# Optimization experiments

Hardware: AMD Instinct MI355X
Metric: run time of the kernel (lower is better)

## Reference

```python
import jax, jax.numpy as jnp
import numpy as np

EPS = 1e-5  # BatchNorm2d default eps


def _squash(s, axis):
    # s * (|s|^2 / ((1+|s|^2) * |s|)) == s * |s| / (1 + |s|^2)
    n = jnp.linalg.norm(s, axis=axis, keepdims=True)
    return s * (n / (1.0 + n * n))


def _bn(y, g, b, m, v):
    # eval-mode batchnorm with running stats, broadcast over channel axis
    return (y - m) * (g * jax.lax.rsqrt(v + EPS)) + b


def setup_inputs() -> dict:
    key = jax.random.key(0)
    ks = jax.random.split(key, 18)
    B, N = 4, 2048
    f32 = jnp.float32
    return {
        "x": jax.random.normal(ks[0], (B, N, 3), f32),
        "w1": 0.1 * jax.random.normal(ks[1], (64, 3), f32),
        "g1": jax.random.uniform(ks[2], (64,), f32) + 0.5,
        "b1": 0.1 * jax.random.normal(ks[3], (64,), f32),
        "m1": 0.1 * jax.random.normal(ks[4], (64,), f32),
        "v1": jax.random.uniform(ks[5], (64,), f32) + 0.5,
        "w2": 0.05 * jax.random.normal(ks[6], (128, 64), f32),
        "g2": jax.random.uniform(ks[7], (128,), f32) + 0.5,
        "b2": 0.1 * jax.random.normal(ks[8], (128,), f32),
        "m2": 0.1 * jax.random.normal(ks[9], (128,), f32),
        "v2": jax.random.uniform(ks[10], (128,), f32) + 0.5,
        "wb": 0.05 * jax.random.normal(ks[11], (16, 1024, 128), f32),
        "gb": jax.random.uniform(ks[12], (16, 1024), f32) + 0.5,
        "bb": 0.1 * jax.random.normal(ks[13], (16, 1024), f32),
        "mb": 0.1 * jax.random.normal(ks[14], (16, 1024), f32),
        "vb": jax.random.uniform(ks[15], (16, 1024), f32) + 0.5,
        "Wc": 0.01 * jax.random.normal(ks[16], (32, 1024, 16, 32), f32),
    }


def reference(x, w1, g1, b1, m1, v1, w2, g2, b2, m2, v2,
              wb, gb, bb, mb, vb, Wc):
    # shared MLP: 1x1 convs over points -> plain matmuls, channels-last
    h = jax.nn.relu(_bn(jnp.einsum('bnc,oc->bno', x, w1), g1, b1, m1, v1))   # [B,N,64]
    h = jax.nn.relu(_bn(jnp.einsum('bnc,oc->bno', h, w2), g2, b2, m2, v2))   # [B,N,128]

    # 16 independent branches batched into one einsum: [B,16,N,1024]
    y = jnp.einsum('bnc,koc->bkno', h, wb)
    y = _bn(y, gb[:, None, :], bb[:, None, :], mb[:, None, :], vb[:, None, :])
    feat = jnp.max(y, axis=2)                 # maxpool over N -> [B,16,1024]

    # concat along capsule dim: capsules [B,1024,16] (vec dim = branch index)
    caps = _squash(jnp.swapaxes(feat, 1, 2), axis=2)

    # Capsule: u[b,o,i,v] = caps[b,i,:] @ Wc[o,i,:,:]  -> [B,32,1024,32]
    u = jnp.einsum('bie,oiev->boiv', caps, Wc)
    u_d = jax.lax.stop_gradient(u)
    b_log = jnp.zeros(u.shape[:3] + (1,), u.dtype)  # routing logits [B,32,1024,1]
    T = 3
    s = None
    for i in range(T):
        c = jax.nn.softmax(b_log, axis=1)
        if i == T - 1:
            s = jnp.sum(u * c, axis=2)                       # [B,32,32]
        else:
            a = _squash(jnp.sum(u * c, axis=2), axis=2)      # [B,32,32]
            agree = jnp.sum(a[:, :, None, :] * u_d, axis=3, keepdims=True)
            b_log = b_log + agree
    return _squash(s, axis=2)                                # [B,32,32]
```

## Files before the change

### kernel.cpp

```cpp
#include <hip/hip_runtime.h>
#include <math.h>

typedef float f32x4 __attribute__((ext_vector_type(4)));
typedef short bf16x8 __attribute__((ext_vector_type(8)));

#define BN_EPS 1e-5f

__device__ __forceinline__ unsigned short bf16_hi(float v, float& rem) {
  unsigned int u = __float_as_uint(v);
  unsigned int r = u + 0x7FFFu + ((u >> 16) & 1u);
  unsigned short h = (unsigned short)(r >> 16);
  rem = v - __uint_as_float((unsigned int)h << 16);
  return h;
}
__device__ __forceinline__ unsigned short bf16_rne(float v) {
  unsigned int u = __float_as_uint(v);
  unsigned int r = u + 0x7FFFu + ((u >> 16) & 1u);
  return (unsigned short)(r >> 16);
}

__global__ __launch_bounds__(256) void k0_wbsplit(
    const float* __restrict__ wb,
    unsigned short* __restrict__ wbh, unsigned short* __restrict__ wbm)
{
  int i = (blockIdx.x * 256 + threadIdx.x) * 4;
  f32x4 v = *(const f32x4*)(wb + i);
  unsigned short h[4], m[4];
  #pragma unroll
  for (int q = 0; q < 4; ++q) {
    float rem;
    h[q] = bf16_hi(v[q], rem);
    m[q] = bf16_rne(rem);
  }
  typedef unsigned short u16x4 __attribute__((ext_vector_type(4)));
  u16x4 vh = {h[0], h[1], h[2], h[3]};
  u16x4 vm = {m[0], m[1], m[2], m[3]};
  *(u16x4*)(wbh + i) = vh;
  *(u16x4*)(wbm + i) = vm;
}

__global__ __launch_bounds__(256) void k1_mlp(
    const float* __restrict__ x,
    const float* __restrict__ w1, const float* __restrict__ g1,
    const float* __restrict__ b1, const float* __restrict__ m1,
    const float* __restrict__ v1,
    const float* __restrict__ w2, const float* __restrict__ g2,
    const float* __restrict__ b2, const float* __restrict__ m2,
    const float* __restrict__ v2,
    unsigned short* __restrict__ h2h, unsigned short* __restrict__ h2m)
{
  __shared__ float w1s[64 * 3];
  __shared__ float s1c[64], o1c[64];
  __shared__ float w2s[64 * 132];
  __shared__ float s2c[128], o2c[128];
  __shared__ float h1s[64 * 64];

  const int tid = threadIdx.x;
  const int b = blockIdx.x >> 5;
  const int n0 = (blockIdx.x & 31) << 6;

  if (tid < 64) {
    float s = g1[tid] / sqrtf(v1[tid] + BN_EPS);
    s1c[tid] = s;
    o1c[tid] = b1[tid] - m1[tid] * s;
    w1s[tid * 3 + 0] = w1[tid * 3 + 0];
    w1s[tid * 3 + 1] = w1[tid * 3 + 1];
    w1s[tid * 3 + 2] = w1[tid * 3 + 2];
  }
  if (tid < 128) {
    float s = g2[tid] / sqrtf(v2[tid] + BN_EPS);
    s2c[tid] = s;
    o2c[tid] = b2[tid] - m2[tid] * s;
  }
  for (int it = 0; it < 32; ++it) {
    int idx = tid + (it << 8);
    int o = idx & 63, j = idx >> 6;
    w2s[o * 132 + j] = w2[j * 64 + o];
  }
  __syncthreads();

  const int n = tid & 63, half = tid >> 6;

  const float* xp = x + ((size_t)(b << 11) + n0 + n) * 3;
  float xv0 = xp[0], xv1 = xp[1], xv2 = xp[2];
  for (int oo = 0; oo < 16; ++oo) {
    int o = (half << 4) + oo;
    float d = xv0 * w1s[o * 3] + xv1 * w1s[o * 3 + 1] + xv2 * w1s[o * 3 + 2];
    d = d * s1c[o] + o1c[o];
    h1s[o * 64 + n] = fmaxf(d, 0.f);
  }
  __syncthreads();

  float acc[32];
  #pragma unroll
  for (int jj = 0; jj < 32; ++jj) acc[jj] = 0.f;
  const int j0 = half << 5;
  for (int o = 0; o < 64; ++o) {
    float a = h1s[o * 64 + n];
    const f32x4* wrow = (const f32x4*)&w2s[o * 132 + j0];
    #pragma unroll
    for (int jg = 0; jg < 8; ++jg) {
      f32x4 wv = wrow[jg];
      acc[jg * 4 + 0] = fmaf(a, wv[0], acc[jg * 4 + 0]);
      acc[jg * 4 + 1] = fmaf(a, wv[1], acc[jg * 4 + 1]);
      acc[jg * 4 + 2] = fmaf(a, wv[2], acc[jg * 4 + 2]);
      acc[jg * 4 + 3] = fmaf(a, wv[3], acc[jg * 4 + 3]);
    }
  }
  const size_t rowbase = ((size_t)(b << 11) + n0 + n) * 128 + j0;
  #pragma unroll
  for (int q = 0; q < 4; ++q) {
    bf16x8 vh, vm;
    #pragma unroll
    for (int e = 0; e < 8; ++e) {
      int jj = q * 8 + e;
      int j = j0 + jj;
      float vl = fmaxf(acc[jj] * s2c[j] + o2c[j], 0.f);
      float rem;
      unsigned short hh = bf16_hi(vl, rem);
      vh[e] = (short)hh;
      vm[e] = (short)bf16_rne(rem);
    }
    *(bf16x8*)(h2h + rowbase + q * 8) = vh;
    *(bf16x8*)(h2m + rowbase + q * 8) = vm;
  }
}

__global__ __launch_bounds__(256, 2) void k2_mfma(
    const unsigned short* __restrict__ h2h,
    const unsigned short* __restrict__ h2m,
    const unsigned short* __restrict__ wbh,
    const unsigned short* __restrict__ wbm,
    float* __restrict__ feat)
{
  __shared__ unsigned short Wl[2][16384];
  __shared__ float redm[4][128];

  const int tid = threadIdx.x;
  const int ot = blockIdx.x & 7;
  const int p = blockIdx.x >> 3;
  const int k = p & 15, b = p >> 4;
  const int o0 = ot << 7;

  {
    const size_t base = ((size_t)(k << 10) + o0) * 128;
    for (int ver = 0; ver < 2; ++ver) {
      const unsigned short* src = (ver ? wbm : wbh) + base;
      for (int it = 0; it < 8; ++it) {
        int c = tid + (it << 8);
        int l15 = c & 15, l4 = (c >> 4) & 3, ks = (c >> 6) & 3, ot2 = c >> 8;
        int o = (ot2 << 4) + l15, kk = (ks << 5) + (l4 << 3);
        bf16x8 v = *(const bf16x8*)(src + (size_t)o * 128 + kk);
        *(bf16x8*)(&Wl[ver][c << 3]) = v;
      }
    }
  }
  __syncthreads();

  const int lane = tid & 63, w = tid >> 6;
  const int l15 = lane & 15, l4 = lane >> 4;

  const size_t abase = (size_t)b * 2048 * 128 + (size_t)l15 * 128 + l4 * 8;
  const unsigned short* pah = h2h + abase;
  const unsigned short* pam = h2m + abase;

  float mxv[8];
  #pragma unroll
  for (int j = 0; j < 8; ++j) mxv[j] = -3.4e38f;

  for (int itn = 0; itn < 16; ++itn) {
    const int n0 = (itn << 7) + (w << 5);
    const unsigned short* ph = pah + (size_t)n0 * 128;
    const unsigned short* pm = pam + (size_t)n0 * 128;

    f32x4 acc[2][8];
    #pragma unroll
    for (int r = 0; r < 2; ++r)
      #pragma unroll
      for (int j = 0; j < 8; ++j) {
        f32x4 z = {0.f, 0.f, 0.f, 0.f};
        acc[r][j] = z;
      }

    #pragma unroll
    for (int ks = 0; ks < 4; ++ks) {
      bf16x8 ah0 = *(const bf16x8*)(ph + (ks << 5));
      bf16x8 ah1 = *(const bf16x8*)(ph + 2048 + (ks << 5));
      bf16x8 am0 = *(const bf16x8*)(pm + (ks << 5));
      bf16x8 am1 = *(const bf16x8*)(pm + 2048 + (ks << 5));
      #pragma unroll
      for (int ot2 = 0; ot2 < 8; ++ot2) {
        const int cb = (((ot2 << 2) + ks) << 9) + (lane << 3);
        bf16x8 bh = *(const bf16x8*)(&Wl[0][cb]);
        bf16x8 bm = *(const bf16x8*)(&Wl[1][cb]);
        acc[0][ot2] = __builtin_amdgcn_mfma_f32_16x16x32_bf16(ah0, bh, acc[0][ot2], 0, 0, 0);
        acc[1][ot2] = __builtin_amdgcn_mfma_f32_16x16x32_bf16(ah1, bh, acc[1][ot2], 0, 0, 0);
        acc[0][ot2] = __builtin_amdgcn_mfma_f32_16x16x32_bf16(ah0, bm, acc[0][ot2], 0, 0, 0);
        acc[1][ot2] = __builtin_amdgcn_mfma_f32_16x16x32_bf16(ah1, bm, acc[1][ot2], 0, 0, 0);
        acc[0][ot2] = __builtin_amdgcn_mfma_f32_16x16x32_bf16(am0, bh, acc[0][ot2], 0, 0, 0);
        acc[1][ot2] = __builtin_amdgcn_mfma_f32_16x16x32_bf16(am1, bh, acc[1][ot2], 0, 0, 0);
      }
    }
    #pragma unroll
    for (int ot2 = 0; ot2 < 8; ++ot2) {
      #pragma unroll
      for (int r = 0; r < 2; ++r) {
        f32x4 a4 = acc[r][ot2];
        mxv[ot2] = fmaxf(mxv[ot2],
                         fmaxf(fmaxf(a4[0], a4[1]), fmaxf(a4[2], a4[3])));
      }
    }
  }

  #pragma unroll
  for (int ot2 = 0; ot2 < 8; ++ot2) {
    float m = mxv[ot2];
    m = fmaxf(m, __shfl_xor(m, 16));
    m = fmaxf(m, __shfl_xor(m, 32));
    mxv[ot2] = m;
  }
  if (lane < 16) {
    #pragma unroll
    for (int ot2 = 0; ot2 < 8; ++ot2) redm[w][(ot2 << 4) + lane] = mxv[ot2];
  }
  __syncthreads();
  if (tid < 128) {
    float m = fmaxf(fmaxf(redm[0][tid], redm[1][tid]),
                    fmaxf(redm[2][tid], redm[3][tid]));
    feat[((size_t)(b * 16 + k) << 10) + o0 + tid] = m;
  }
}

__global__ __launch_bounds__(256) void k3a_caps(
    const float* __restrict__ feat,
    const float* __restrict__ gb, const float* __restrict__ bb,
    const float* __restrict__ mb, const float* __restrict__ vb,
    float* __restrict__ caps)
{
  int g = blockIdx.x * 256 + threadIdx.x;
  int b = g >> 10, i = g & 1023;
  float val[16];
  float ss = 0.f;
  #pragma unroll
  for (int e = 0; e < 16; ++e) {
    int ei = (e << 10) + i;
    float f = feat[((size_t)(b << 4) << 10) + ei];
    float sc = gb[ei] / sqrtf(vb[ei] + BN_EPS);
    float vv = (f - mb[ei]) * sc + bb[ei];
    val[e] = vv;
    ss += vv * vv;
  }
  float nrm = sqrtf(ss);
  float scl = nrm / (1.f + nrm * nrm);
  f32x4* cp = (f32x4*)&caps[(size_t)((b << 10) + i) << 4];
  #pragma unroll
  for (int q = 0; q < 4; ++q) {
    f32x4 v;
    v[0] = val[q * 4 + 0] * scl; v[1] = val[q * 4 + 1] * scl;
    v[2] = val[q * 4 + 2] * scl; v[3] = val[q * 4 + 3] * scl;
    cp[q] = v;
  }
}

__global__ __launch_bounds__(256) void k3b_u(
    const float* __restrict__ caps, const float* __restrict__ Wc,
    float* __restrict__ u, float* __restrict__ s0p)
{
  __shared__ float caps_l[4 * 32 * 16];
  __shared__ float s_red[16 * 32];

  const int tid = threadIdx.x;
  const int o = blockIdx.x & 31, it = blockIdx.x >> 5;
  const int i0 = it << 5;

  for (int ld = 0; ld < 8; ++ld) {
    int idx = tid + (ld << 8);
    int bq = idx >> 9, il = (idx >> 4) & 31, e = idx & 15;
    caps_l[idx] = caps[(size_t)(((bq << 10) + i0 + il) << 4) + e];
  }
  __syncthreads();

  const int w = tid >> 6, lane = tid & 63;
  const int eh = lane >> 5, v = lane & 31;
  float s0acc[4] = {0.f, 0.f, 0.f, 0.f};

  for (int ii = 0; ii < 8; ++ii) {
    int il = (w << 3) + ii;
    int i = i0 + il;
    const float* wc = Wc + ((size_t)(o << 10) + i) * 512 + (eh << 8) + v;
    float acc[4] = {0.f, 0.f, 0.f, 0.f};
    #pragma unroll
    for (int ee = 0; ee < 8; ++ee) {
      float wv = wc[ee * 32];
      int e = (eh << 3) + ee;
      #pragma unroll
      for (int bq = 0; bq < 4; ++bq)
        acc[bq] = fmaf(caps_l[bq * 512 + il * 16 + e], wv, acc[bq]);
    }
    #pragma unroll
    for (int bq = 0; bq < 4; ++bq) {
      acc[bq] += __shfl_xor(acc[bq], 32);
      if (eh == 0) {
        u[(size_t)((((bq << 5) + o) << 10) + i) * 32 + v] = acc[bq];
        s0acc[bq] += acc[bq];
      }
    }
  }
  if (eh == 0) {
    #pragma unroll
    for (int bq = 0; bq < 4; ++bq) s_red[((w << 2) + bq) * 32 + v] = s0acc[bq];
  }
  __syncthreads();
  if (tid < 128) {
    int bq = tid >> 5, vv = tid & 31;
    float s = s_red[bq * 32 + vv] + s_red[(4 + bq) * 32 + vv] +
              s_red[(8 + bq) * 32 + vv] + s_red[(12 + bq) * 32 + vv];
    s0p[(size_t)(((bq << 5) + it) << 5 | o) * 32 + vv] = s;
  }
}

__global__ __launch_bounds__(256) void k4_squash(
    const float* __restrict__ sp, float* __restrict__ out, float prescale)
{
  const int tid = threadIdx.x;
  const int b = blockIdx.x;
  const int o = tid >> 3, vq = (tid & 7) << 2;
  f32x4 acc = {0.f, 0.f, 0.f, 0.f};
  for (int it = 0; it < 32; ++it) {
    f32x4 p = *(const f32x4*)(sp + (size_t)(((b << 5) + it) << 5 | o) * 32 + vq);
    acc += p;
  }
  acc *= prescale;
  float ss = acc[0] * acc[0] + acc[1] * acc[1] + acc[2] * acc[2] + acc[3] * acc[3];
  ss += __shfl_xor(ss, 1);
  ss += __shfl_xor(ss, 2);
  ss += __shfl_xor(ss, 4);
  float nrm = sqrtf(ss);
  float scl = nrm / (1.f + nrm * nrm);
  f32x4 r = acc * scl;
  *(f32x4*)(out + (size_t)((b << 5) + o) * 32 + vq) = r;
}

__global__ __launch_bounds__(256) void k5_route(
    const float* __restrict__ u, const float* __restrict__ aprev,
    const float* __restrict__ bprev, float* __restrict__ bout,
    float* __restrict__ spart, int pass)
{
  __shared__ float a_l[32 * 33];
  __shared__ float u_l[4 * 32 * 33];
  __shared__ float s_red[4 * 32 * 33];

  const int tid = threadIdx.x;
  const int b = blockIdx.x >> 5, it = blockIdx.x & 31;
  const int i0 = it << 5;

  for (int ld = 0; ld < 4; ++ld) {
    int idx = tid + (ld << 8);
    int o = idx >> 5, v = idx & 31;
    a_l[o * 33 + v] = aprev[((b << 5) + o) * 32 + v];
  }
  __syncthreads();

  const int w = tid >> 6, lane = tid & 63;
  const int ln5 = lane & 31, hb = lane >> 5;
  float* uw = &u_l[w * 1056];

  float sacc[16];
  #pragma unroll
  for (int q = 0; q < 16; ++q) sacc[q] = 0.f;

  for (int ii = 0; ii < 8; ++ii) {
    int i = i0 + (w << 3) + ii;
    #pragma unroll
    for (int rr = 0; rr < 16; ++rr) {
      int o = (rr << 1) + hb;
      uw[o * 33 + ln5] = u[(size_t)((((b << 5) + o) << 10) + i) * 32 + ln5];
    }
    float ag = 0.f;
    #pragma unroll
    for (int q = 0; q < 16; ++q) {
      int vv = (hb << 4) + q;
      ag = fmaf(a_l[ln5 * 33 + vv], uw[ln5 * 33 + vv], ag);
    }
    ag += __shfl_xor(ag, 32);
    float bl = ag;
    if (pass == 1) bl += bprev[(((b << 5) + ln5) << 10) + i];
    if (pass == 0 && hb == 0) bout[(((b << 5) + ln5) << 10) + i] = bl;
    float m = bl;
    m = fmaxf(m, __shfl_xor(m, 1));
    m = fmaxf(m, __shfl_xor(m, 2));
    m = fmaxf(m, __shfl_xor(m, 4));
    m = fmaxf(m, __shfl_xor(m, 8));
    m = fmaxf(m, __shfl_xor(m, 16));
    float e = expf(bl - m);
    float sm = e;
    sm += __shfl_xor(sm, 1);
    sm += __shfl_xor(sm, 2);
    sm += __shfl_xor(sm, 4);
    sm += __shfl_xor(sm, 8);
    sm += __shfl_xor(sm, 16);
    float c = e / sm;
    #pragma unroll
    for (int q = 0; q < 16; ++q) {
      int vv = (hb << 4) + q;
      sacc[q] = fmaf(c, uw[ln5 * 33 + vv], sacc[q]);
    }
  }
  #pragma unroll
  for (int q = 0; q < 16; ++q)
    s_red[w * 1056 + ln5 * 33 + (hb << 4) + q] = sacc[q];
  __syncthreads();
  for (int ld = 0; ld < 4; ++ld) {
    int idx = tid + (ld << 8);
    int o = idx >> 5, vv = idx & 31;
    float s = s_red[o * 33 + vv] + s_red[1056 + o * 33 + vv] +
              s_red[2112 + o * 33 + vv] + s_red[3168 + o * 33 + vv];
    spart[(size_t)(((b << 5) + it) << 5 | o) * 32 + vv] = s;
  }
}

extern "C" void kernel_launch(void* const* d_in, const int* in_sizes, int n_in,
                              void* d_out, int out_size, void* d_ws, size_t ws_size,
                              hipStream_t stream) {
  const float* x  = (const float*)d_in[0];
  const float* w1 = (const float*)d_in[1];
  const float* g1 = (const float*)d_in[2];
  const float* b1 = (const float*)d_in[3];
  const float* m1 = (const float*)d_in[4];
  const float* v1 = (const float*)d_in[5];
  const float* w2 = (const float*)d_in[6];
  const float* g2 = (const float*)d_in[7];
  const float* b2 = (const float*)d_in[8];
  const float* m2 = (const float*)d_in[9];
  const float* v2 = (const float*)d_in[10];
  const float* wb = (const float*)d_in[11];
  const float* gb = (const float*)d_in[12];
  const float* bb = (const float*)d_in[13];
  const float* mb = (const float*)d_in[14];
  const float* vb = (const float*)d_in[15];
  const float* Wc = (const float*)d_in[16];
  float* out = (float*)d_out;
  float* ws = (float*)d_ws;

  unsigned short* h2h = (unsigned short*)(ws);
  unsigned short* h2m = (unsigned short*)(ws + 524288);
  unsigned short* wbh = (unsigned short*)(ws + 1048576);
  unsigned short* wbm = (unsigned short*)(ws + 2097152);
  float* u    = ws;
  float* feat = ws + 4194304;
  float* caps = ws + 4259840;
  float* s0p  = ws + 4325376;
  float* s1p  = ws + 4456448;
  float* s2p  = ws + 4587520;
  float* a0   = ws + 4718592;
  float* a1   = ws + 4722688;
  float* b1l  = ws + 4726784;

  k0_wbsplit<<<2048, 256, 0, stream>>>(wb, wbh, wbm);
  k1_mlp<<<128, 256, 0, stream>>>(x, w1, g1, b1, m1, v1,
                                  w2, g2, b2, m2, v2, h2h, h2m);
  k2_mfma<<<512, 256, 0, stream>>>(h2h, h2m, wbh, wbm, feat);
  k3a_caps<<<16, 256, 0, stream>>>(feat, gb, bb, mb, vb, caps);
  k3b_u<<<1024, 256, 0, stream>>>(caps, Wc, u, s0p);
  k4_squash<<<4, 256, 0, stream>>>(s0p, a0, 1.f / 32.f);
  k5_route<<<128, 256, 0, stream>>>(u, a0, b1l, b1l, s1p, 0);
  k4_squash<<<4, 256, 0, stream>>>(s1p, a1, 1.f);
  k5_route<<<128, 256, 0, stream>>>(u, a1, b1l, b1l, s2p, 1);
  k4_squash<<<4, 256, 0, stream>>>(s2p, out, 1.f);
}
```

Baseline: 392.3 us.

## Remap k2 blocks per XCD and double-buffer A-fragment global loads

The block index is remapped so that blocks landing on the same XCD (bid&7) share a batch index, and the split-bf16 activation rows for that batch are reused in that XCD's L2. The A-operand global loads are double-buffered in registers, with the next k-slice (and the next n-tile) prefetched while MFMAs run on the current fragments. This targets global-load latency stalls in the main MFMA loop. It costs extra VGPRs, which may pressure occupancy at launch bounds (256,2), and the prefetch logic adds indexing complexity.

```diff
diff --git a/kernel.cpp b/kernel.cpp
--- a/kernel.cpp
+++ b/kernel.cpp
@@ -137,9 +137,12 @@
   __shared__ float redm[4][128];
 
   const int tid = threadIdx.x;
-  const int ot = blockIdx.x & 7;
-  const int p = blockIdx.x >> 3;
-  const int k = p & 15, b = p >> 4;
+  const int bid = blockIdx.x;
+  const int xcd = bid & 7;
+  const int rest = bid >> 3;
+  const int b = xcd >> 1;
+  const int k = rest & 15;
+  const int ot = ((xcd & 1) << 2) + (rest >> 4);
   const int o0 = ot << 7;
 
   {
@@ -168,10 +171,18 @@
   #pragma unroll
   for (int j = 0; j < 8; ++j) mxv[j] = -3.4e38f;
 
+  bf16x8 f0[4], f1[4];
+  {
+    const size_t so = (size_t)(w << 5) * 128;
+    f0[0] = *(const bf16x8*)(pah + so);
+    f0[1] = *(const bf16x8*)(pah + so + 2048);
+    f0[2] = *(const bf16x8*)(pam + so);
+    f0[3] = *(const bf16x8*)(pam + so + 2048);
+  }
+
   for (int itn = 0; itn < 16; ++itn) {
-    const int n0 = (itn << 7) + (w << 5);
-    const unsigned short* ph = pah + (size_t)n0 * 128;
-    const unsigned short* pm = pam + (size_t)n0 * 128;
+    const size_t so = ((size_t)(itn << 7) + (w << 5)) * 128;
+    const size_t sn = (itn < 15) ? so + 128 * 128 : so;
 
     f32x4 acc[2][8];
     #pragma unroll
@@ -183,24 +194,48 @@
       }
 
     #pragma unroll
-    for (int ks = 0; ks < 4; ++ks) {
-      bf16x8 ah0 = *(const bf16x8*)(ph + (ks << 5));
-      bf16x8 ah1 = *(const bf16x8*)(ph + 2048 + (ks << 5));
-      bf16x8 am0 = *(const bf16x8*)(pm + (ks << 5));
-      bf16x8 am1 = *(const bf16x8*)(pm + 2048 + (ks << 5));
+    for (int kp = 0; kp < 2; ++kp) {
+      const int ksA = kp << 1, ksB = ksA + 1;
+      {
+        const size_t sp = so + (ksB << 5);
+        f1[0] = *(const bf16x8*)(pah + sp);
+        f1[1] = *(const bf16x8*)(pah + sp + 2048);
+        f1[2] = *(const bf16x8*)(pam + sp);
+        f1[3] = *(const bf16x8*)(pam + sp + 2048);
+      }
       #pragma unroll
       for (int ot2 = 0; ot2 < 8; ++ot2) {
-        const int cb = (((ot2 << 2) + ks) << 9) + (lane << 3);
+        const int cb = (((ot2 << 2) + ksA) << 9) + (lane << 3);
         bf16x8 bh = *(const bf16x8*)(&Wl[0][cb]);
         bf16x8 bm = *(const bf16x8*)(&Wl[1][cb]);
-        acc[0][ot2] = __builtin_amdgcn_mfma_f32_16x16x32_bf16(ah0, bh, acc[0][ot2], 0, 0, 0);
-        acc[1][ot2] = __builtin_amdgcn_mfma_f32_16x16x32_bf16(ah1, bh, acc[1][ot2], 0, 0, 0);
-        acc[0][ot2] = __builtin_amdgcn_mfma_f32_16x16x32_bf16(ah0, bm, acc[0][ot2], 0, 0, 0);
-        acc[1][ot2] = __builtin_amdgcn_mfma_f32_16x16x32_bf16(ah1, bm, acc[1][ot2], 0, 0, 0);
-        acc[0][ot2] = __builtin_amdgcn_mfma_f32_16x16x32_bf16(am0, bh, acc[0][ot2], 0, 0, 0);
-        acc[1][ot2] = __builtin_amdgcn_mfma_f32_16x16x32_bf16(am1, bh, acc[1][ot2], 0, 0, 0);
-      }
-    }
+        acc[0][ot2] = __builtin_amdgcn_mfma_f32_16x16x32_bf16(f0[0], bh, acc[0][ot2], 0, 0, 0);
+        acc[1][ot2] = __builtin_amdgcn_mfma_f32_16x16x32_bf16(f0[1], bh, acc[1][ot2], 0, 0, 0);
+        acc[0][ot2] = __builtin_amdgcn_mfma_f32_16x16x32_bf16(f0[0], bm, acc[0][ot2], 0, 0, 0);
+        acc[1][ot2] = __builtin_amdgcn_mfma_f32_16x16x32_bf16(f0[1], bm, acc[1][ot2], 0, 0, 0);
+        acc[0][ot2] = __builtin_amdgcn_mfma_f32_16x16x32_bf16(f0[2], bh, acc[0][ot2], 0, 0, 0);
+        acc[1][ot2] = __builtin_amdgcn_mfma_f32_16x16x32_bf16(f0[3], bh, acc[1][ot2], 0, 0, 0);
+      }
+      {
+        const size_t sp = (kp == 0) ? (so + 64) : sn;
+        f0[0] = *(const bf16x8*)(pah + sp);
+        f0[1] = *(const bf16x8*)(pah + sp + 2048);
+        f0[2] = *(const bf16x8*)(pam + sp);
+        f0[3] = *(const bf16x8*)(pam + sp + 2048);
+      }
+      #pragma unroll
+      for (int ot2 = 0; ot2 < 8; ++ot2) {
+        const int cb = (((ot2 << 2) + ksB) << 9) + (lane << 3);
+        bf16x8 bh = *(const bf16x8*)(&Wl[0][cb]);
+        bf16x8 bm = *(const bf16x8*)(&Wl[1][cb]);
+        acc[0][ot2] = __builtin_amdgcn_mfma_f32_16x16x32_bf16(f1[0], bh, acc[0][ot2], 0, 0, 0);
+        acc[1][ot2] = __builtin_amdgcn_mfma_f32_16x16x32_bf16(f1[1], bh, acc[1][ot2], 0, 0, 0);
+        acc[0][ot2] = __builtin_amdgcn_mfma_f32_16x16x32_bf16(f1[0], bm, acc[0][ot2], 0, 0, 0);
+        acc[1][ot2] = __builtin_amdgcn_mfma_f32_16x16x32_bf16(f1[1], bm, acc[1][ot2], 0, 0, 0);
+        acc[0][ot2] = __builtin_amdgcn_mfma_f32_16x16x32_bf16(f1[2], bh, acc[0][ot2], 0, 0, 0);
+        acc[1][ot2] = __builtin_amdgcn_mfma_f32_16x16x32_bf16(f1[3], bh, acc[1][ot2], 0, 0, 0);
+      }
+    }
+
     #pragma unroll
     for (int ot2 = 0; ot2 < 8; ++ot2) {
       #pragma unroll
```

Result: faster. 381.8 us (-2.7%).

## Pre-swizzle bf16 split operands, process two branches per block with register prefetch

Applied to the files above, without the earlier changes.

The weight-split and MLP kernels now write hi/lo bf16 parts interleaved in the exact MFMA fragment layout, so loads into the main GEMM become contiguous 16-byte chunks. The GEMM kernel handles two branches per block, reusing each activation fragment across both, which halves activation reads and the grid size. Weights are staged into LDS with async global-to-LDS loads, and activation fragments are software-prefetched one k-step ahead. The costs are double the LDS per block (occupancy bound lowered to 1) and much higher register pressure from four accumulator sets, and only 256 blocks to spread across the CUs.

```diff
diff --git a/kernel.cpp b/kernel.cpp
--- a/kernel.cpp
+++ b/kernel.cpp
@@ -19,24 +19,38 @@
   return (unsigned short)(r >> 16);
 }
 
+__device__ __forceinline__ void async_ld16(const unsigned short* g,
+                                           unsigned short* l) {
+  __builtin_amdgcn_global_load_lds(
+      (const __attribute__((address_space(1))) void*)g,
+      (__attribute__((address_space(3))) void*)l, 16, 0, 0);
+}
+
+
 __global__ __launch_bounds__(256) void k0_wbsplit(
-    const float* __restrict__ wb,
-    unsigned short* __restrict__ wbh, unsigned short* __restrict__ wbm)
-{
-  int i = (blockIdx.x * 256 + threadIdx.x) * 4;
-  f32x4 v = *(const f32x4*)(wb + i);
-  unsigned short h[4], m[4];
-  #pragma unroll
-  for (int q = 0; q < 4; ++q) {
+    const float* __restrict__ wb, unsigned short* __restrict__ wbf)
+{
+  int g = blockIdx.x * 256 + threadIdx.x;
+  int l15 = g & 15, l4 = (g >> 4) & 3, kkb = (g >> 6) & 3;
+  int ot16 = (g >> 8) & 63, k = g >> 14;
+
+  const float* src = wb + ((size_t)((k << 10) + (ot16 << 4) + l15)) * 128 +
+                     (kkb << 5) + (l4 << 3);
+  f32x4 v0 = *(const f32x4*)(src);
+  f32x4 v1 = *(const f32x4*)(src + 4);
+
+  bf16x8 vh, vm;
+  #pragma unroll
+  for (int e = 0; e < 8; ++e) {
+    float x = (e < 4) ? v0[e] : v1[e - 4];
     float rem;
-    h[q] = bf16_hi(v[q], rem);
-    m[q] = bf16_rne(rem);
-  }
-  typedef unsigned short u16x4 __attribute__((ext_vector_type(4)));
-  u16x4 vh = {h[0], h[1], h[2], h[3]};
-  u16x4 vm = {m[0], m[1], m[2], m[3]};
-  *(u16x4*)(wbh + i) = vh;
-  *(u16x4*)(wbm + i) = vm;
+    vh[e] = (short)bf16_hi(x, rem);
+    vm[e] = (short)bf16_rne(rem);
+  }
+  const int chunk = (k << 9) + (ot16 << 3) + (kkb << 1);
+  unsigned short* dst = wbf + ((size_t)chunk << 9) + ((g & 63) << 3);
+  *(bf16x8*)(dst) = vh;
+  *(bf16x8*)(dst + 512) = vm;
 }
 
 __global__ __launch_bounds__(256) void k1_mlp(
@@ -47,7 +61,7 @@
     const float* __restrict__ w2, const float* __restrict__ g2,
     const float* __restrict__ b2, const float* __restrict__ m2,
     const float* __restrict__ v2,
-    unsigned short* __restrict__ h2h, unsigned short* __restrict__ h2m)
+    unsigned short* __restrict__ h2f)
 {
   __shared__ float w1s[64 * 3];
   __shared__ float s1c[64], o1c[64];
@@ -107,127 +121,153 @@
       acc[jg * 4 + 3] = fmaf(a, wv[3], acc[jg * 4 + 3]);
     }
   }
-  const size_t rowbase = ((size_t)(b << 11) + n0 + n) * 128 + j0;
-  #pragma unroll
-  for (int q = 0; q < 4; ++q) {
+  const int gn = n0 + n;
+  const int t = gn >> 4, rr = gn & 15;
+  const size_t cb = ((size_t)((b * 128 + t) * 4 + half)) << 10;
+  #pragma unroll
+  for (int l4 = 0; l4 < 4; ++l4) {
     bf16x8 vh, vm;
     #pragma unroll
     for (int e = 0; e < 8; ++e) {
-      int jj = q * 8 + e;
+      int jj = l4 * 8 + e;
       int j = j0 + jj;
       float vl = fmaxf(acc[jj] * s2c[j] + o2c[j], 0.f);
       float rem;
-      unsigned short hh = bf16_hi(vl, rem);
-      vh[e] = (short)hh;
+      vh[e] = (short)bf16_hi(vl, rem);
       vm[e] = (short)bf16_rne(rem);
     }
-    *(bf16x8*)(h2h + rowbase + q * 8) = vh;
-    *(bf16x8*)(h2m + rowbase + q * 8) = vm;
-  }
-}
-
-__global__ __launch_bounds__(256, 2) void k2_mfma(
-    const unsigned short* __restrict__ h2h,
-    const unsigned short* __restrict__ h2m,
-    const unsigned short* __restrict__ wbh,
-    const unsigned short* __restrict__ wbm,
+    *(bf16x8*)(h2f + cb + (l4 << 7) + (rr << 3)) = vh;
+    *(bf16x8*)(h2f + cb + 512 + (l4 << 7) + (rr << 3)) = vm;
+  }
+}
+
+#define MFMA16(a, bv, c) __builtin_amdgcn_mfma_f32_16x16x32_bf16(a, bv, c, 0, 0, 0)
+
+#define LOADP(V0, V1, V2, V3, IT, KS) {                                        \
+  const unsigned short* _p = gA + (((size_t)(((IT) << 3) + (w << 1))) << 12) + \
+                             ((KS) << 10) + (lane << 3);                       \
+  V0 = *(const bf16x8*)(_p);                                                   \
+  V1 = *(const bf16x8*)(_p + 512);                                             \
+  V2 = *(const bf16x8*)(_p + 4096);                                            \
+  V3 = *(const bf16x8*)(_p + 4096 + 512); }
+
+#define PHASE(Ah0, Am0, Ah1, Am1, KS)                                          \
+  _Pragma("unroll")                                                            \
+  for (int ot2 = 0; ot2 < 8; ++ot2) {                                          \
+    const int cb = (((ot2 << 3) + ((KS) << 1)) << 9) + (lane << 3);            \
+    bf16x8 b0h = *(const bf16x8*)(&Wl[0][cb]);                                 \
+    bf16x8 b0m = *(const bf16x8*)(&Wl[0][cb + 512]);                           \
+    bf16x8 b1h = *(const bf16x8*)(&Wl[1][cb]);                                 \
+    bf16x8 b1m = *(const bf16x8*)(&Wl[1][cb + 512]);                           \
+    acc00[ot2] = MFMA16(Ah0, b0h, acc00[ot2]);                                 \
+    acc01[ot2] = MFMA16(Ah1, b0h, acc01[ot2]);                                 \
+    acc10[ot2] = MFMA16(Ah0, b1h, acc10[ot2]);                                 \
+    acc11[ot2] = MFMA16(Ah1, b1h, acc11[ot2]);                                 \
+    acc00[ot2] = MFMA16(Ah0, b0m, acc00[ot2]);                                 \
+    acc01[ot2] = MFMA16(Ah1, b0m, acc01[ot2]);                                 \
+    acc10[ot2] = MFMA16(Ah0, b1m, acc10[ot2]);                                 \
+    acc11[ot2] = MFMA16(Ah1, b1m, acc11[ot2]);                                 \
+    acc00[ot2] = MFMA16(Am0, b0h, acc00[ot2]);                                 \
+    acc01[ot2] = MFMA16(Am1, b0h, acc01[ot2]);                                 \
+    acc10[ot2] = MFMA16(Am0, b1h, acc10[ot2]);                                 \
+    acc11[ot2] = MFMA16(Am1, b1h, acc11[ot2]);                                 \
+  }
+
+__global__ __launch_bounds__(256, 1) void k2_mfma(
+    const unsigned short* __restrict__ h2f,
+    const unsigned short* __restrict__ wbf,
     float* __restrict__ feat)
 {
-  __shared__ unsigned short Wl[2][16384];
-  __shared__ float redm[4][128];
+  __shared__ unsigned short Wl[2][32768];
+  __shared__ float redm[2][4][128];
 
   const int tid = threadIdx.x;
-  const int ot = blockIdx.x & 7;
-  const int p = blockIdx.x >> 3;
-  const int k = p & 15, b = p >> 4;
+  const int bid = blockIdx.x;
+  const int ot = bid & 7;
+  const int kp = (bid >> 3) & 7;
+  const int b  = bid >> 6;
   const int o0 = ot << 7;
-
-  {
-    const size_t base = ((size_t)(k << 10) + o0) * 128;
-    for (int ver = 0; ver < 2; ++ver) {
-      const unsigned short* src = (ver ? wbm : wbh) + base;
-      for (int it = 0; it < 8; ++it) {
-        int c = tid + (it << 8);
-        int l15 = c & 15, l4 = (c >> 4) & 3, ks = (c >> 6) & 3, ot2 = c >> 8;
-        int o = (ot2 << 4) + l15, kk = (ks << 5) + (l4 << 3);
-        bf16x8 v = *(const bf16x8*)(src + (size_t)o * 128 + kk);
-        *(bf16x8*)(&Wl[ver][c << 3]) = v;
-      }
-    }
-  }
-  __syncthreads();
-
   const int lane = tid & 63, w = tid >> 6;
-  const int l15 = lane & 15, l4 = lane >> 4;
-
-  const size_t abase = (size_t)b * 2048 * 128 + (size_t)l15 * 128 + l4 * 8;
-  const unsigned short* pah = h2h + abase;
-  const unsigned short* pam = h2m + abase;
-
-  float mxv[8];
-  #pragma unroll
-  for (int j = 0; j < 8; ++j) mxv[j] = -3.4e38f;
+
+  #pragma unroll
+  for (int kk = 0; kk < 2; ++kk) {
+    const unsigned short* src =
+        wbf + ((size_t)((((kp << 1) + kk) << 9) + (ot << 6)) << 9);
+    for (int it = 0; it < 16; ++it) {
+      int seg = (it << 2) + w;
+      async_ld16(src + (seg << 9) + (lane << 3), &Wl[kk][seg << 9]);
+    }
+  }
+
+  const unsigned short* gA = h2f + ((size_t)b << 19);
+
+  bf16x8 P00, P01, P02, P03, P10, P11, P12, P13;
+  bf16x8 P20, P21, P22, P23, P30, P31, P32, P33;
+  LOADP(P00, P01, P02, P03, 0, 0);
+  LOADP(P10, P11, P12, P13, 0, 1);
+
+  float mx0[8], mx1[8];
+  #pragma unroll
+  for (int j = 0; j < 8; ++j) { mx0[j] = -3.4e38f; mx1[j] = -3.4e38f; }
+
+  __syncthreads();
 
   for (int itn = 0; itn < 16; ++itn) {
-    const int n0 = (itn << 7) + (w << 5);
-    const unsigned short* ph = pah + (size_t)n0 * 128;
-    const unsigned short* pm = pam + (size_t)n0 * 128;
-
-    f32x4 acc[2][8];
-    #pragma unroll
-    for (int r = 0; r < 2; ++r)
-      #pragma unroll
-      for (int j = 0; j < 8; ++j) {
-        f32x4 z = {0.f, 0.f, 0.f, 0.f};
-        acc[r][j] = z;
-      }
-
-    #pragma unroll
-    for (int ks = 0; ks < 4; ++ks) {
-      bf16x8 ah0 = *(const bf16x8*)(ph + (ks << 5));
-      bf16x8 ah1 = *(const bf16x8*)(ph + 2048 + (ks << 5));
-      bf16x8 am0 = *(const bf16x8*)(pm + (ks << 5));
-      bf16x8 am1 = *(const bf16x8*)(pm + 2048 + (ks << 5));
-      #pragma unroll
-      for (int ot2 = 0; ot2 < 8; ++ot2) {
-        const int cb = (((ot2 << 2) + ks) << 9) + (lane << 3);
-        bf16x8 bh = *(const bf16x8*)(&Wl[0][cb]);
-        bf16x8 bm = *(const bf16x8*)(&Wl[1][cb]);
-        acc[0][ot2] = __builtin_amdgcn_mfma_f32_16x16x32_bf16(ah0, bh, acc[0][ot2], 0, 0, 0);
-        acc[1][ot2] = __builtin_amdgcn_mfma_f32_16x16x32_bf16(ah1, bh, acc[1][ot2], 0, 0, 0);
-        acc[0][ot2] = __builtin_amdgcn_mfma_f32_16x16x32_bf16(ah0, bm, acc[0][ot2], 0, 0, 0);
-        acc[1][ot2] = __builtin_amdgcn_mfma_f32_16x16x32_bf16(ah1, bm, acc[1][ot2], 0, 0, 0);
-        acc[0][ot2] = __builtin_amdgcn_mfma_f32_16x16x32_bf16(am0, bh, acc[0][ot2], 0, 0, 0);
-        acc[1][ot2] = __builtin_amdgcn_mfma_f32_16x16x32_bf16(am1, bh, acc[1][ot2], 0, 0, 0);
-      }
-    }
+    const int tn = (itn < 15) ? itn + 1 : 15;
+
+    f32x4 acc00[8], acc01[8], acc10[8], acc11[8];
+    #pragma unroll
+    for (int j = 0; j < 8; ++j) {
+      f32x4 z = {0.f, 0.f, 0.f, 0.f};
+      acc00[j] = z; acc01[j] = z; acc10[j] = z; acc11[j] = z;
+    }
+
+    LOADP(P20, P21, P22, P23, itn, 2);
+    PHASE(P00, P01, P02, P03, 0);
+    LOADP(P30, P31, P32, P33, itn, 3);
+    PHASE(P10, P11, P12, P13, 1);
+    LOADP(P00, P01, P02, P03, tn, 0);
+    PHASE(P20, P21, P22, P23, 2);
+    LOADP(P10, P11, P12, P13, tn, 1);
+    PHASE(P30, P31, P32, P33, 3);
+
     #pragma unroll
     for (int ot2 = 0; ot2 < 8; ++ot2) {
-      #pragma unroll
-      for (int r = 0; r < 2; ++r) {
-        f32x4 a4 = acc[r][ot2];
-        mxv[ot2] = fmaxf(mxv[ot2],
-                         fmaxf(fmaxf(a4[0], a4[1]), fmaxf(a4[2], a4[3])));
-      }
+      f32x4 a = acc00[ot2], c = acc01[ot2];
+      float m0 = fmaxf(fmaxf(a[0], a[1]), fmaxf(a[2], a[3]));
+      float m1 = fmaxf(fmaxf(c[0], c[1]), fmaxf(c[2], c[3]));
+      mx0[ot2] = fmaxf(mx0[ot2], fmaxf(m0, m1));
+      f32x4 d = acc10[ot2], e = acc11[ot2];
+      float m2 = fmaxf(fmaxf(d[0], d[1]), fmaxf(d[2], d[3]));
+      float m3 = fmaxf(fmaxf(e[0], e[1]), fmaxf(e[2], e[3]));
+      mx1[ot2] = fmaxf(mx1[ot2], fmaxf(m2, m3));
     }
   }
 
   #pragma unroll
   for (int ot2 = 0; ot2 < 8; ++ot2) {
-    float m = mxv[ot2];
+    float m = mx0[ot2];
     m = fmaxf(m, __shfl_xor(m, 16));
     m = fmaxf(m, __shfl_xor(m, 32));
-    mxv[ot2] = m;
+    mx0[ot2] = m;
+    float q = mx1[ot2];
+    q = fmaxf(q, __shfl_xor(q, 16));
+    q = fmaxf(q, __shfl_xor(q, 32));
+    mx1[ot2] = q;
   }
   if (lane < 16) {
     #pragma unroll
-    for (int ot2 = 0; ot2 < 8; ++ot2) redm[w][(ot2 << 4) + lane] = mxv[ot2];
-  }
-  __syncthreads();
-  if (tid < 128) {
-    float m = fmaxf(fmaxf(redm[0][tid], redm[1][tid]),
-                    fmaxf(redm[2][tid], redm[3][tid]));
-    feat[((size_t)(b * 16 + k) << 10) + o0 + tid] = m;
+    for (int ot2 = 0; ot2 < 8; ++ot2) {
+      redm[0][w][(ot2 << 4) + lane] = mx0[ot2];
+      redm[1][w][(ot2 << 4) + lane] = mx1[ot2];
+    }
+  }
+  __syncthreads();
+  {
+    int kk = tid >> 7, o = tid & 127;
+    float m = fmaxf(fmaxf(redm[kk][0][o], redm[kk][1][o]),
+                    fmaxf(redm[kk][2][o], redm[kk][3][o]));
+    feat[((size_t)(b * 16 + (kp << 1) + kk) << 10) + o0 + o] = m;
   }
 }
 
@@ -442,10 +482,8 @@
   float* out = (float*)d_out;
   float* ws = (float*)d_ws;
 
-  unsigned short* h2h = (unsigned short*)(ws);
-  unsigned short* h2m = (unsigned short*)(ws + 524288);
-  unsigned short* wbh = (unsigned short*)(ws + 1048576);
-  unsigned short* wbm = (unsigned short*)(ws + 2097152);
+  unsigned short* h2f = (unsigned short*)(ws);
+  unsigned short* wbf = (unsigned short*)(ws + 1048576);
   float* u    = ws;
   float* feat = ws + 4194304;
   float* caps = ws + 4259840;
@@ -456,10 +494,10 @@
   float* a1   = ws + 4722688;
   float* b1l  = ws + 4726784;
 
-  k0_wbsplit<<<2048, 256, 0, stream>>>(wb, wbh, wbm);
+  k0_wbsplit<<<1024, 256, 0, stream>>>(wb, wbf);
   k1_mlp<<<128, 256, 0, stream>>>(x, w1, g1, b1, m1, v1,
-                                  w2, g2, b2, m2, v2, h2h, h2m);
-  k2_mfma<<<512, 256, 0, stream>>>(h2h, h2m, wbh, wbm, feat);
+                                  w2, g2, b2, m2, v2, h2f);
+  k2_mfma<<<256, 256, 0, stream>>>(h2f, wbf, feat);
   k3a_caps<<<16, 256, 0, stream>>>(feat, gb, bb, mb, vb, caps);
   k3b_u<<<1024, 256, 0, stream>>>(caps, Wc, u, s0p);
   k4_squash<<<4, 256, 0, stream>>>(s0p, a0, 1.f / 32.f);
```

Result: slower. 479.5 us (+22.2%).
